# Kernel tuning notes

Measured on AMD Instinct MI355X. Metric: run time of the kernel, lower is better.

Reference implementation:

```python
import jax, jax.numpy as jnp
import numpy as np

N = 50000      # nodes
E = 800000     # edges
FIN = 128      # num_feature
EDIM = 16      # edge_dim
OUT = 64       # out_dim (per-head channels; concat=False averages heads)
H = 4          # heads
SCALE = 1.0 / float(np.sqrt(OUT))


def _layernorm(h, g, b):
    mu = h.mean(-1, keepdims=True)
    var = ((h - mu) ** 2).mean(-1, keepdims=True)
    return (h - mu) * jax.lax.rsqrt(var + 1e-5) * g + b


def _tconv(x, src, dst, ea, Wq, bq, Wk, bk, Wv, bv, We, Ws, bs):
    # PyG TransformerConv, concat=False, root_weight=True, eval mode (no dropout)
    n = x.shape[0]
    q = (x @ Wq + bq).reshape(n, H, OUT)[dst]   # [E,H,D] query at destination
    k = (x @ Wk + bk).reshape(n, H, OUT)[src]   # [E,H,D] key at source
    v = (x @ Wv + bv).reshape(n, H, OUT)[src]   # [E,H,D] value at source
    e = (ea @ We).reshape(-1, H, OUT)           # [E,H,D] edge embedding (no bias)
    logits = jnp.einsum('ehd,ehd->eh', q, k + e) * SCALE   # [E,H]
    # segment softmax over incoming edges of each destination node
    m = jax.lax.stop_gradient(jax.ops.segment_max(logits, dst, num_segments=n))
    a = jnp.exp(logits - m[dst])
    s = jax.ops.segment_sum(a, dst, num_segments=n)
    alpha = a / s[dst]                                     # [E,H]
    agg = jax.ops.segment_sum((v + e) * alpha[..., None], dst, num_segments=n)  # [N,H,D]
    return agg.mean(axis=1) + x @ Ws + bs      # concat=False -> head mean; + skip


def _forward(x, src, dst, ea, p1, p2, p3, g, b):
    h = x
    for p in (p1, p2, p3):
        h = jax.nn.gelu(_layernorm(_tconv(h, src, dst, ea, *p), g, b), approximate=False)
    return h


def setup_inputs() -> dict:
    key = jax.random.key(0)
    ks = iter(jax.random.split(key, 64))
    def nrm(shp, s=0.05):
        return jax.random.normal(next(ks), shp, jnp.float32) * s
    inp = {
        'x': nrm((N, FIN), 1.0),
        'edge_index': jax.random.randint(next(ks), (2, E), 0, N),
        'edge_attr': nrm((E, EDIM), 1.0),
    }
    for l, fin in ((1, FIN), (2, OUT), (3, OUT)):
        inp[f'Wq{l}'] = nrm((fin, H * OUT)); inp[f'bq{l}'] = jnp.zeros((H * OUT,), jnp.float32)
        inp[f'Wk{l}'] = nrm((fin, H * OUT)); inp[f'bk{l}'] = jnp.zeros((H * OUT,), jnp.float32)
        inp[f'Wv{l}'] = nrm((fin, H * OUT)); inp[f'bv{l}'] = jnp.zeros((H * OUT,), jnp.float32)
        inp[f'We{l}'] = nrm((EDIM, H * OUT))
        inp[f'Ws{l}'] = nrm((fin, OUT)); inp[f'bs{l}'] = jnp.zeros((OUT,), jnp.float32)
    inp['ln_g'] = jnp.ones((OUT,), jnp.float32)
    inp['ln_b'] = jnp.zeros((OUT,), jnp.float32)
    return inp


def reference(x, edge_index, edge_attr,
              Wq1, bq1, Wk1, bk1, Wv1, bv1, We1, Ws1, bs1,
              Wq2, bq2, Wk2, bk2, Wv2, bv2, We2, Ws2, bs2,
              Wq3, bq3, Wk3, bk3, Wv3, bv3, We3, Ws3, bs3,
              ln_g, ln_b):
    src, dst = edge_index[0], edge_index[1]
    p1 = (Wq1, bq1, Wk1, bk1, Wv1, bv1, We1, Ws1, bs1)
    p2 = (Wq2, bq2, Wk2, bk2, Wv2, bv2, We2, Ws2, bs2)
    p3 = (Wq3, bq3, Wk3, bk3, Wv3, bv3, We3, Ws3, bs3)
    return _forward(x, src, dst, edge_attr, p1, p2, p3, ln_g, ln_b)
```

## Files before the change

kernel.cpp:

```cpp
#include <hip/hip_runtime.h>
#include <hip/hip_bf16.h>
#include <math.h>

#define NNODES 50000
#define NEDGES 800000
#define HD     256
#define CW     640
#define NTOT   896

typedef __hip_bfloat16 bf16;
typedef unsigned short u16;
typedef unsigned char  u8;
typedef unsigned int   u32;
typedef __attribute__((ext_vector_type(8))) short bf16x8;
typedef __attribute__((ext_vector_type(4))) float f32x4;
typedef __attribute__((ext_vector_type(2))) float f32x2;

__device__ __forceinline__ float lo16f(u32 u) { return __uint_as_float(u << 16); }
__device__ __forceinline__ float hi16f(u32 u) { return __uint_as_float(u & 0xFFFF0000u); }
__device__ __forceinline__ short f2s(float v) { __hip_bfloat16 h = __float2bfloat16(v); return *(short*)&h; }

template<int CTRL>
__device__ __forceinline__ float dppadd(float x) {
    int t = __builtin_amdgcn_update_dpp(0, __float_as_int(x), CTRL, 0xF, 0xF, true);
    return x + __int_as_float(t);
}

__global__ void hist_kernel(const int* __restrict__ dst, int* __restrict__ deg, int E) {
    int e = blockIdx.x * 256 + threadIdx.x;
    if (e < E) atomicAdd(&deg[dst[e]], 1);
}

__global__ void scanA(const int* __restrict__ deg, int* __restrict__ locincl,
                      int* __restrict__ blocksum, int n) {
    int tid = threadIdx.x;
    int i = blockIdx.x * 256 + tid;
    int v = (i < n) ? deg[i] : 0;
    int lane = tid & 63, w = tid >> 6;
    int s = v;
    #pragma unroll
    for (int off = 1; off < 64; off <<= 1) {
        int t = __shfl_up(s, off);
        if (lane >= off) s += t;
    }
    __shared__ int wsum[4];
    if (lane == 63) wsum[w] = s;
    __syncthreads();
    for (int ww = 0; ww < w; ww++) s += wsum[ww];
    if (i < n) locincl[i] = s;
    if (tid == 255) blocksum[blockIdx.x] = s;
}

__global__ void scanB(const int* __restrict__ blocksum, int* __restrict__ blockoff,
                      int nb, int* __restrict__ rowptr, int n) {
    int tid = threadIdx.x;
    int v = (tid < nb) ? blocksum[tid] : 0;
    int lane = tid & 63, w = tid >> 6;
    int s = v;
    #pragma unroll
    for (int off = 1; off < 64; off <<= 1) {
        int t = __shfl_up(s, off);
        if (lane >= off) s += t;
    }
    __shared__ int wsum[4];
    if (lane == 63) wsum[w] = s;
    __syncthreads();
    for (int ww = 0; ww < w; ww++) s += wsum[ww];
    if (tid < nb) blockoff[tid] = s - v;
    if (tid == 255) rowptr[n] = s;
}

__global__ void scanC(const int* __restrict__ deg, const int* __restrict__ locincl,
                      const int* __restrict__ blockoff,
                      int* __restrict__ rowptr, int* __restrict__ cursor, int n) {
    int i = blockIdx.x * 256 + threadIdx.x;
    if (i < n) {
        int ex = locincl[i] - deg[i] + blockoff[blockIdx.x];
        rowptr[i] = ex;
        cursor[i] = ex;
    }
}

__global__ void scatter_kernel(const int* __restrict__ src, const int* __restrict__ dst,
                               int* __restrict__ cursor, int2* __restrict__ csr2, int E) {
    int e = blockIdx.x * 256 + threadIdx.x;
    if (e < E) {
        int d = dst[e];
        int p = atomicAdd(&cursor[d], 1);
        csr2[p] = make_int2(src[e], e);
    }
}

__global__ void pack_all(const float* __restrict__ Wq, const float* __restrict__ bq,
                         const float* __restrict__ Wk, const float* __restrict__ bk,
                         const float* __restrict__ Wv, const float* __restrict__ bv,
                         const float* __restrict__ We,
                         const float* __restrict__ Ws, const float* __restrict__ bs,
                         bf16* __restrict__ Wc, float* __restrict__ b, int K) {
    int n = blockIdx.x, c = threadIdx.x;
    float v, bb;
    if (n < 256)      { v = Wq[(size_t)c * 256 + n];         bb = bq[n]; }
    else if (n < 320) {
        int t = n - 256, h = t >> 4, j = t & 15;
        float s = 0.f, sb = 0.f;
        #pragma unroll 8
        for (int d = 0; d < 64; d++) {
            float wv = We[j * HD + h * 64 + d];
            s += Wq[(size_t)c * 256 + h * 64 + d] * wv;
            sb += bq[h * 64 + d] * wv;
        }
        v = s; bb = sb;
    }
    else if (n < 576) { v = Wv[(size_t)c * 256 + (n - 320)]; bb = bv[n - 320]; }
    else if (n < 640) { v = Ws[(size_t)c * 64  + (n - 576)]; bb = bs[n - 576]; }
    else              { v = Wk[(size_t)c * 256 + (n - 640)]; bb = bk[n - 640]; }
    Wc[(size_t)n * K + c] = __float2bfloat16(v);
    if (c == 0) b[n] = bb;
}

template<typename TA, int K>
__global__ void __launch_bounds__(256) gemm_fused(
    const TA* __restrict__ A, const bf16* __restrict__ Wc, const float* __restrict__ bias,
    bf16* __restrict__ comb, u8* __restrict__ k8)
{
    constexpr int KS  = K / 32;
    constexpr int CPR = K / 8;
    __shared__ short Bl[64 * K];
    int tid = threadIdx.x, w = tid >> 6, lane = tid & 63;
    int cl = lane & 15, aq = lane >> 4;
    int m = blockIdx.x * 64 + w * 16 + cl;
    int rowc = (m < NNODES) ? m : (NNODES - 1);

    bf16x8 af[KS];
    if constexpr (sizeof(TA) == 4) {
        const float* ar = (const float*)A + (size_t)rowc * K;
        #pragma unroll
        for (int ks = 0; ks < KS; ks++) {
            const float4* ap = (const float4*)(ar + ks * 32 + aq * 8);
            float4 f0 = ap[0], f1 = ap[1];
            union { short s[8]; bf16x8 v; } t;
            t.s[0] = f2s(f0.x); t.s[1] = f2s(f0.y); t.s[2] = f2s(f0.z); t.s[3] = f2s(f0.w);
            t.s[4] = f2s(f1.x); t.s[5] = f2s(f1.y); t.s[6] = f2s(f1.z); t.s[7] = f2s(f1.w);
            af[ks] = t.v;
        }
    } else {
        const u16* ar = (const u16*)A + (size_t)rowc * K;
        #pragma unroll
        for (int ks = 0; ks < KS; ks++) af[ks] = *(const bf16x8*)(ar + ks * 32 + aq * 8);
    }

    for (int chunk = 0; chunk < 14; chunk++) {
        int n0 = chunk * 64;
        __syncthreads();
        #pragma unroll
        for (int p = 0; p < CPR / 4; p++) {
            int slot = tid + p * 256;
            int row = slot / CPR, j = slot % CPR;
            *(uint4*)&Bl[row * K + ((j ^ (row & 7)) << 3)] =
                *(const uint4*)((const u16*)Wc + (size_t)(n0 + row) * K + (j << 3));
        }
        __syncthreads();

        f32x4 acc[4] = {};
        #pragma unroll
        for (int t = 0; t < 4; t++) {
            #pragma unroll
            for (int ks = 0; ks < KS; ks++) {
                int g = ((ks * 4 + aq) ^ (cl & 7)) << 3;
                bf16x8 bfr = *(const bf16x8*)&Bl[(t * 16 + cl) * K + g];
                acc[t] = __builtin_amdgcn_mfma_f32_16x16x32_bf16(bfr, af[ks], acc[t], 0, 0, 0);
            }
        }

        if (m < NNODES) {
            #pragma unroll
            for (int t = 0; t < 4; t++) {
                float4 bv = *(const float4*)&bias[n0 + t * 16 + aq * 4];
                float v0 = acc[t][0] + bv.x, v1 = acc[t][1] + bv.y;
                float v2 = acc[t][2] + bv.z, v3 = acc[t][3] + bv.w;
                if (chunk < 10) {
                    u32 lo = (u32)(u16)f2s(v0) | ((u32)(u16)f2s(v1) << 16);
                    u32 hi = (u32)(u16)f2s(v2) | ((u32)(u16)f2s(v3) << 16);
                    *(uint2*)((u16*)comb + (size_t)m * CW + n0 + t * 16 + aq * 4) = make_uint2(lo, hi);
                } else {
                    u32 pk = __builtin_amdgcn_cvt_pk_fp8_f32(v0, v1, 0, false);
                    pk = __builtin_amdgcn_cvt_pk_fp8_f32(v2, v3, pk, true);
                    *(u32*)(k8 + (size_t)m * 256 + (n0 - 640) + t * 16 + aq * 4) = pk;
                }
            }
        }
    }
}

__device__ __forceinline__ void edge_accum(
    u32 s, u32 eid,
    const char* __restrict__ comb_b, const char* __restrict__ k8_b, const char* __restrict__ eattr_b,
    u32 koff, u32 voff, u32 eoff,
    float qf0, float qf1, float qf2, float qf3, float qwe_r,
    float& ss, float& av0, float& av1, float& av2, float& av3, float& ae)
{
    u32   kw = *(const u32*)  (k8_b   + ((s << 8) + koff));
    uint2 vw = *(const uint2*)(comb_b + (s * 1280u + voff));
    float ea = *(const float*)(eattr_b + ((eid << 6) + eoff));
    f32x2 k01 = __builtin_amdgcn_cvt_pk_f32_fp8(kw, false);
    f32x2 k23 = __builtin_amdgcn_cvt_pk_f32_fp8(kw, true);
    float part = qf0 * k01[0] + qf1 * k01[1] + qf2 * k23[0] + qf3 * k23[1] + qwe_r * ea;
    part = dppadd<0xB1>(part);
    part = dppadd<0x4E>(part);
    part = dppadd<0x141>(part);
    part = dppadd<0x140>(part);
    float alpha = __expf(part * 0.125f);
    ss += alpha;
    ae += alpha * ea;
    av0 += alpha * lo16f(vw.x); av1 += alpha * hi16f(vw.x);
    av2 += alpha * lo16f(vw.y); av3 += alpha * hi16f(vw.y);
}

__global__ void __launch_bounds__(256) node_fused(
    const int* __restrict__ rowptr, const int2* __restrict__ csr2,
    const float* __restrict__ eattr, const u16* __restrict__ comb,
    const u8* __restrict__ k8, const float* __restrict__ We,
    const float* __restrict__ lng, const float* __restrict__ lnb,
    bf16* __restrict__ outB, float* __restrict__ outF)
{
    int tid = threadIdx.x, w = tid >> 6, lane = tid & 63;
    int n = blockIdx.x * 4 + w;
    int hg = lane >> 4, j16 = lane & 15, coff = 4 * lane;
    __shared__ float sAV[4][256];
    __shared__ float sAE[4][64];

    const u16* crow = comb + (size_t)n * CW;
    uint2 qv = *(const uint2*)(crow + coff);
    float qf0 = lo16f(qv.x), qf1 = hi16f(qv.x), qf2 = lo16f(qv.y), qf3 = hi16f(qv.y);
    float qwe_r = __uint_as_float((u32)crow[256 + lane] << 16);

    const char* comb_b  = (const char*)comb;
    const char* k8_b    = (const char*)k8;
    const char* eattr_b = (const char*)eattr;
    u32 koff = (u32)coff;
    u32 voff = 640u + ((u32)coff << 1);
    u32 eoff = (u32)j16 << 2;

    int e0 = rowptr[n], e1 = rowptr[n + 1];
    float ss = 0.f, av0 = 0.f, av1 = 0.f, av2 = 0.f, av3 = 0.f, ae = 0.f;

    for (int base = e0; base < e1; base += 64) {
        int cnt = e1 - base; if (cnt > 64) cnt = 64;
        int2 meta = make_int2(0, 0);
        if (lane < cnt) meta = csr2[base + lane];
        int i = 0;
        for (; i + 3 < cnt; i += 4) {
            u32 s0 = __builtin_amdgcn_readlane(meta.x, i);
            u32 q0 = __builtin_amdgcn_readlane(meta.y, i);
            u32 s1 = __builtin_amdgcn_readlane(meta.x, i + 1);
            u32 q1 = __builtin_amdgcn_readlane(meta.y, i + 1);
            u32 s2 = __builtin_amdgcn_readlane(meta.x, i + 2);
            u32 q2 = __builtin_amdgcn_readlane(meta.y, i + 2);
            u32 s3 = __builtin_amdgcn_readlane(meta.x, i + 3);
            u32 q3 = __builtin_amdgcn_readlane(meta.y, i + 3);
            edge_accum(s0, q0, comb_b, k8_b, eattr_b, koff, voff, eoff, qf0, qf1, qf2, qf3, qwe_r, ss, av0, av1, av2, av3, ae);
            edge_accum(s1, q1, comb_b, k8_b, eattr_b, koff, voff, eoff, qf0, qf1, qf2, qf3, qwe_r, ss, av0, av1, av2, av3, ae);
            edge_accum(s2, q2, comb_b, k8_b, eattr_b, koff, voff, eoff, qf0, qf1, qf2, qf3, qwe_r, ss, av0, av1, av2, av3, ae);
            edge_accum(s3, q3, comb_b, k8_b, eattr_b, koff, voff, eoff, qf0, qf1, qf2, qf3, qwe_r, ss, av0, av1, av2, av3, ae);
        }
        for (; i < cnt; ++i) {
            u32 s0 = __builtin_amdgcn_readlane(meta.x, i);
            u32 q0 = __builtin_amdgcn_readlane(meta.y, i);
            edge_accum(s0, q0, comb_b, k8_b, eattr_b, koff, voff, eoff, qf0, qf1, qf2, qf3, qwe_r, ss, av0, av1, av2, av3, ae);
        }
    }

    float inv = (ss > 0.f) ? 1.f / ss : 0.f;
    *(float4*)&sAV[w][coff] = make_float4(av0 * inv, av1 * inv, av2 * inv, av3 * inv);
    sAE[w][lane] = ae * inv;

    int d = lane;
    float val = 0.f;
    #pragma unroll
    for (int h = 0; h < 4; h++) {
        float xv = sAV[w][h * 64 + d];
        #pragma unroll
        for (int j = 0; j < 16; j++) xv += sAE[w][h * 16 + j] * We[j * HD + h * 64 + d];
        val += xv;
    }
    val = val * 0.25f + __uint_as_float((u32)crow[576 + d] << 16);

    float m = val;
    #pragma unroll
    for (int off = 1; off < 64; off <<= 1) m += __shfl_xor(m, off);
    m *= (1.f / 64.f);
    float diff = val - m;
    float vr = diff * diff;
    #pragma unroll
    for (int off = 1; off < 64; off <<= 1) vr += __shfl_xor(vr, off);
    vr *= (1.f / 64.f);
    float y = diff * rsqrtf(vr + 1e-5f) * lng[d] + lnb[d];
    float ge = 0.5f * y * (1.f + erff(y * 0.70710678118654752f));
    if (outF) outF[(size_t)n * 64 + d] = ge;
    else      outB[(size_t)n * 64 + d] = __float2bfloat16(ge);
}

extern "C" void kernel_launch(void* const* d_in, const int* in_sizes, int n_in,
                              void* d_out, int out_size, void* d_ws, size_t ws_size,
                              hipStream_t stream)
{
    const float* x     = (const float*)d_in[0];
    const int*   eidx  = (const int*)d_in[1];
    const float* eattr = (const float*)d_in[2];
    struct P { const float *Wq,*bq,*Wk,*bk,*Wv,*bv,*We,*Ws,*bs; };
    P p[3];
    for (int l = 0; l < 3; l++) {
        int base = 3 + l * 9;
        p[l].Wq = (const float*)d_in[base + 0]; p[l].bq = (const float*)d_in[base + 1];
        p[l].Wk = (const float*)d_in[base + 2]; p[l].bk = (const float*)d_in[base + 3];
        p[l].Wv = (const float*)d_in[base + 4]; p[l].bv = (const float*)d_in[base + 5];
        p[l].We = (const float*)d_in[base + 6];
        p[l].Ws = (const float*)d_in[base + 7]; p[l].bs = (const float*)d_in[base + 8];
    }
    const float* lng = (const float*)d_in[30];
    const float* lnb = (const float*)d_in[31];

    char* ws = (char*)d_ws;
    size_t off = 0;
    auto alloc = [&](size_t bytes) { void* pp = ws + off; off += (bytes + 255) & ~(size_t)255; return pp; };
    int*   rowptr   = (int*)  alloc((NNODES + 1) * 4);
    int*   cursor   = (int*)  alloc(NNODES * 4);
    int*   deg      = (int*)  alloc(NNODES * 4);
    int*   blocksum = (int*)  alloc(256 * 4);
    int*   blockoff = (int*)  alloc(256 * 4);
    int2*  csr2     = (int2*) alloc((size_t)NEDGES * 8);
    bf16*  hbuf     = (bf16*) alloc((size_t)NNODES * 64 * 2);
    bf16*  comb     = (bf16*) alloc((size_t)NNODES * CW * 2);
    u8*    k8       = (u8*)   alloc((size_t)NNODES * 256);
    bf16*  Wc       = (bf16*) alloc((size_t)NTOT * 128 * 2);
    float* b896     = (float*)alloc(NTOT * 4);
    (void)ws_size;

    const int* srcArr = eidx;
    const int* dstArr = eidx + NEDGES;

    int NB = (NNODES + 255) / 256;
    (void)hipMemsetAsync(deg, 0, NNODES * 4, stream);
    hist_kernel<<<(NEDGES + 255) / 256, 256, 0, stream>>>(dstArr, deg, NEDGES);
    scanA<<<NB, 256, 0, stream>>>(deg, cursor, blocksum, NNODES);
    scanB<<<1, 256, 0, stream>>>(blocksum, blockoff, NB, rowptr, NNODES);
    scanC<<<NB, 256, 0, stream>>>(deg, cursor, blockoff, rowptr, cursor, NNODES);
    scatter_kernel<<<(NEDGES + 255) / 256, 256, 0, stream>>>(srcArr, dstArr, cursor, csr2, NEDGES);

    int gm = (NNODES + 63) / 64;
    int fins[3] = {128, 64, 64};

    const void* hin = x;
    for (int l = 0; l < 3; l++) {
        int FIN = fins[l];
        pack_all<<<NTOT, FIN, 0, stream>>>(p[l].Wq, p[l].bq, p[l].Wk, p[l].bk,
                                           p[l].Wv, p[l].bv, p[l].We, p[l].Ws, p[l].bs,
                                           Wc, b896, FIN);
        if (l == 0) gemm_fused<float, 128><<<gm, 256, 0, stream>>>((const float*)hin, Wc, b896, comb, k8);
        else        gemm_fused<bf16,  64><<<gm, 256, 0, stream>>>((const bf16*)hin,  Wc, b896, comb, k8);
        node_fused<<<NNODES / 4, 256, 0, stream>>>(rowptr, csr2, eattr, (const u16*)comb, k8,
            p[l].We, lng, lnb, (l == 2) ? nullptr : hbuf, (l == 2) ? (float*)d_out : nullptr);
        hin = hbuf;
    }
}
```

Measured before the change: 688.5 us.

## Split V into separate buffer, stage GEMM output via LDS, prefetch edges

Moves the value projection into its own contiguous 512-byte-per-node buffer and reorders the combined row so the skip projection sits right after Q and q·We. GEMM epilogue outputs go through a swizzled LDS tile, so each thread issues coalesced 16-byte global stores. The weight chunk for the next step is register-prefetched while the current one computes. The softmax scale and log2(e) are folded into the Q weights so the edge loop can use a raw exp2. The edge loop now reads CSR entries with a rolling 4-edge prefetch instead of wave-wide loads plus readlane broadcasts. This costs extra LDS, one more barrier per chunk and more register pressure.

```diff
diff --git a/kernel.cpp b/kernel.cpp
--- a/kernel.cpp
+++ b/kernel.cpp
@@ -5,13 +5,15 @@
 #define NNODES 50000
 #define NEDGES 800000
 #define HD     256
-#define CW     640
+#define CW     448
 #define NTOT   896
+#define QS     0.18033688011112042f
 
 typedef __hip_bfloat16 bf16;
 typedef unsigned short u16;
 typedef unsigned char  u8;
 typedef unsigned int   u32;
+typedef unsigned long long u64;
 typedef __attribute__((ext_vector_type(8))) short bf16x8;
 typedef __attribute__((ext_vector_type(4))) float f32x4;
 typedef __attribute__((ext_vector_type(2))) float f32x2;
@@ -99,7 +101,7 @@
                          bf16* __restrict__ Wc, float* __restrict__ b, int K) {
     int n = blockIdx.x, c = threadIdx.x;
     float v, bb;
-    if (n < 256)      { v = Wq[(size_t)c * 256 + n];         bb = bq[n]; }
+    if (n < 256)      { v = Wq[(size_t)c * 256 + n] * QS;    bb = bq[n] * QS; }
     else if (n < 320) {
         int t = n - 256, h = t >> 4, j = t & 15;
         float s = 0.f, sb = 0.f;
@@ -109,10 +111,10 @@
             s += Wq[(size_t)c * 256 + h * 64 + d] * wv;
             sb += bq[h * 64 + d] * wv;
         }
-        v = s; bb = sb;
-    }
-    else if (n < 576) { v = Wv[(size_t)c * 256 + (n - 320)]; bb = bv[n - 320]; }
-    else if (n < 640) { v = Ws[(size_t)c * 64  + (n - 576)]; bb = bs[n - 576]; }
+        v = s * QS; bb = sb * QS;
+    }
+    else if (n < 384) { v = Ws[(size_t)c * 64  + (n - 320)]; bb = bs[n - 320]; }
+    else if (n < 640) { v = Wv[(size_t)c * 256 + (n - 384)]; bb = bv[n - 384]; }
     else              { v = Wk[(size_t)c * 256 + (n - 640)]; bb = bk[n - 640]; }
     Wc[(size_t)n * K + c] = __float2bfloat16(v);
     if (c == 0) b[n] = bb;
@@ -121,14 +123,17 @@
 template<typename TA, int K>
 __global__ void __launch_bounds__(256) gemm_fused(
     const TA* __restrict__ A, const bf16* __restrict__ Wc, const float* __restrict__ bias,
-    bf16* __restrict__ comb, u8* __restrict__ k8)
+    bf16* __restrict__ comb, bf16* __restrict__ vbuf, u8* __restrict__ k8)
 {
     constexpr int KS  = K / 32;
     constexpr int CPR = K / 8;
+    constexpr int SLD = CPR / 4;
     __shared__ short Bl[64 * K];
+    __shared__ u8    Tr[64 * 128];
     int tid = threadIdx.x, w = tid >> 6, lane = tid & 63;
     int cl = lane & 15, aq = lane >> 4;
-    int m = blockIdx.x * 64 + w * 16 + cl;
+    int m0 = blockIdx.x * 64;
+    int m  = m0 + w * 16 + cl;
     int rowc = (m < NNODES) ? m : (NNODES - 1);
 
     bf16x8 af[KS];
@@ -149,16 +154,26 @@
         for (int ks = 0; ks < KS; ks++) af[ks] = *(const bf16x8*)(ar + ks * 32 + aq * 8);
     }
 
-    for (int chunk = 0; chunk < 14; chunk++) {
-        int n0 = chunk * 64;
-        __syncthreads();
-        #pragma unroll
-        for (int p = 0; p < CPR / 4; p++) {
+    uint4 sreg[SLD];
+    auto SLOAD = [&](int chunk) {
+        #pragma unroll
+        for (int p = 0; p < SLD; p++) {
             int slot = tid + p * 256;
             int row = slot / CPR, j = slot % CPR;
-            *(uint4*)&Bl[row * K + ((j ^ (row & 7)) << 3)] =
-                *(const uint4*)((const u16*)Wc + (size_t)(n0 + row) * K + (j << 3));
-        }
+            sreg[p] = *(const uint4*)((const u16*)Wc + (size_t)(chunk * 64 + row) * K + (j << 3));
+        }
+    };
+    SLOAD(0);
+
+    for (int chunk = 0; chunk < 14; chunk++) {
+        __syncthreads();
+        #pragma unroll
+        for (int p = 0; p < SLD; p++) {
+            int slot = tid + p * 256;
+            int row = slot / CPR, j = slot % CPR;
+            *(uint4*)&Bl[row * K + ((j ^ (row & 7)) << 3)] = sreg[p];
+        }
+        if (chunk < 13) SLOAD(chunk + 1);
         __syncthreads();
 
         f32x4 acc[4] = {};
@@ -172,55 +187,61 @@
             }
         }
 
-        if (m < NNODES) {
+        int r = w * 16 + cl;
+        if (chunk < 10) {
             #pragma unroll
             for (int t = 0; t < 4; t++) {
-                float4 bv = *(const float4*)&bias[n0 + t * 16 + aq * 4];
-                float v0 = acc[t][0] + bv.x, v1 = acc[t][1] + bv.y;
-                float v2 = acc[t][2] + bv.z, v3 = acc[t][3] + bv.w;
-                if (chunk < 10) {
-                    u32 lo = (u32)(u16)f2s(v0) | ((u32)(u16)f2s(v1) << 16);
-                    u32 hi = (u32)(u16)f2s(v2) | ((u32)(u16)f2s(v3) << 16);
-                    *(uint2*)((u16*)comb + (size_t)m * CW + n0 + t * 16 + aq * 4) = make_uint2(lo, hi);
-                } else {
-                    u32 pk = __builtin_amdgcn_cvt_pk_fp8_f32(v0, v1, 0, false);
-                    pk = __builtin_amdgcn_cvt_pk_fp8_f32(v2, v3, pk, true);
-                    *(u32*)(k8 + (size_t)m * 256 + (n0 - 640) + t * 16 + aq * 4) = pk;
+                float4 bv = *(const float4*)&bias[chunk * 64 + t * 16 + aq * 4];
+                u32 lo = (u32)(u16)f2s(acc[t][0] + bv.x) | ((u32)(u16)f2s(acc[t][1] + bv.y) << 16);
+                u32 hi = (u32)(u16)f2s(acc[t][2] + bv.z) | ((u32)(u16)f2s(acc[t][3] + bv.w) << 16);
+                *(uint2*)&Tr[r * 128 + (((t * 4 + aq) ^ (r & 15)) << 3)] = make_uint2(lo, hi);
+            }
+        } else {
+            #pragma unroll
+            for (int t = 0; t < 4; t++) {
+                float4 bv = *(const float4*)&bias[chunk * 64 + t * 16 + aq * 4];
+                u32 pk = __builtin_amdgcn_cvt_pk_fp8_f32(acc[t][0] + bv.x, acc[t][1] + bv.y, 0, false);
+                pk = __builtin_amdgcn_cvt_pk_fp8_f32(acc[t][2] + bv.z, acc[t][3] + bv.w, pk, true);
+                *(u32*)&Tr[r * 64 + (((t * 4 + aq) ^ (r & 15)) << 2)] = pk;
+            }
+        }
+        __syncthreads();
+
+        int r2 = tid >> 2, q = tid & 3;
+        int gr = m0 + r2;
+        if (gr < NNODES) {
+            if (chunk < 10) {
+                union { u32 d[4]; uint4 v; } o0, o1;
+                #pragma unroll
+                for (int j = 0; j < 4; j++) {
+                    int g = ((q * 4 + j) ^ (r2 & 15)) << 3;
+                    uint2 dv = *(const uint2*)&Tr[r2 * 128 + g];
+                    if (j < 2) { o0.d[2 * j] = dv.x; o0.d[2 * j + 1] = dv.y; }
+                    else       { o1.d[2 * (j - 2)] = dv.x; o1.d[2 * (j - 2) + 1] = dv.y; }
                 }
+                char* dst;
+                if (chunk < 6) dst = (char*)comb + (size_t)gr * (CW * 2) + chunk * 128;
+                else           dst = (char*)vbuf + (size_t)gr * 512 + (chunk - 6) * 128;
+                *(uint4*)(dst + q * 32)      = o0.v;
+                *(uint4*)(dst + q * 32 + 16) = o1.v;
+            } else {
+                union { u32 d[4]; uint4 v; } o;
+                #pragma unroll
+                for (int j = 0; j < 4; j++) {
+                    int g = ((q * 4 + j) ^ (r2 & 15)) << 2;
+                    o.d[j] = *(const u32*)&Tr[r2 * 64 + g];
+                }
+                *(uint4*)((char*)k8 + (size_t)gr * 256 + (chunk - 10) * 64 + q * 16) = o.v;
             }
         }
     }
-}
-
-__device__ __forceinline__ void edge_accum(
-    u32 s, u32 eid,
-    const char* __restrict__ comb_b, const char* __restrict__ k8_b, const char* __restrict__ eattr_b,
-    u32 koff, u32 voff, u32 eoff,
-    float qf0, float qf1, float qf2, float qf3, float qwe_r,
-    float& ss, float& av0, float& av1, float& av2, float& av3, float& ae)
-{
-    u32   kw = *(const u32*)  (k8_b   + ((s << 8) + koff));
-    uint2 vw = *(const uint2*)(comb_b + (s * 1280u + voff));
-    float ea = *(const float*)(eattr_b + ((eid << 6) + eoff));
-    f32x2 k01 = __builtin_amdgcn_cvt_pk_f32_fp8(kw, false);
-    f32x2 k23 = __builtin_amdgcn_cvt_pk_f32_fp8(kw, true);
-    float part = qf0 * k01[0] + qf1 * k01[1] + qf2 * k23[0] + qf3 * k23[1] + qwe_r * ea;
-    part = dppadd<0xB1>(part);
-    part = dppadd<0x4E>(part);
-    part = dppadd<0x141>(part);
-    part = dppadd<0x140>(part);
-    float alpha = __expf(part * 0.125f);
-    ss += alpha;
-    ae += alpha * ea;
-    av0 += alpha * lo16f(vw.x); av1 += alpha * hi16f(vw.x);
-    av2 += alpha * lo16f(vw.y); av3 += alpha * hi16f(vw.y);
 }
 
 __global__ void __launch_bounds__(256) node_fused(
     const int* __restrict__ rowptr, const int2* __restrict__ csr2,
     const float* __restrict__ eattr, const u16* __restrict__ comb,
-    const u8* __restrict__ k8, const float* __restrict__ We,
-    const float* __restrict__ lng, const float* __restrict__ lnb,
+    const u16* __restrict__ vbuf, const u8* __restrict__ k8,
+    const float* __restrict__ We, const float* __restrict__ lng, const float* __restrict__ lnb,
     bf16* __restrict__ outB, float* __restrict__ outF)
 {
     int tid = threadIdx.x, w = tid >> 6, lane = tid & 63;
@@ -234,41 +255,42 @@
     float qf0 = lo16f(qv.x), qf1 = hi16f(qv.x), qf2 = lo16f(qv.y), qf3 = hi16f(qv.y);
     float qwe_r = __uint_as_float((u32)crow[256 + lane] << 16);
 
-    const char* comb_b  = (const char*)comb;
-    const char* k8_b    = (const char*)k8;
-    const char* eattr_b = (const char*)eattr;
-    u32 koff = (u32)coff;
-    u32 voff = 640u + ((u32)coff << 1);
-    u32 eoff = (u32)j16 << 2;
-
-    int e0 = rowptr[n], e1 = rowptr[n + 1];
+    int e0 = __builtin_amdgcn_readfirstlane(rowptr[n]);
+    int e1 = __builtin_amdgcn_readfirstlane(rowptr[n + 1]);
+
     float ss = 0.f, av0 = 0.f, av1 = 0.f, av2 = 0.f, av3 = 0.f, ae = 0.f;
-
-    for (int base = e0; base < e1; base += 64) {
-        int cnt = e1 - base; if (cnt > 64) cnt = 64;
-        int2 meta = make_int2(0, 0);
-        if (lane < cnt) meta = csr2[base + lane];
-        int i = 0;
-        for (; i + 3 < cnt; i += 4) {
-            u32 s0 = __builtin_amdgcn_readlane(meta.x, i);
-            u32 q0 = __builtin_amdgcn_readlane(meta.y, i);
-            u32 s1 = __builtin_amdgcn_readlane(meta.x, i + 1);
-            u32 q1 = __builtin_amdgcn_readlane(meta.y, i + 1);
-            u32 s2 = __builtin_amdgcn_readlane(meta.x, i + 2);
-            u32 q2 = __builtin_amdgcn_readlane(meta.y, i + 2);
-            u32 s3 = __builtin_amdgcn_readlane(meta.x, i + 3);
-            u32 q3 = __builtin_amdgcn_readlane(meta.y, i + 3);
-            edge_accum(s0, q0, comb_b, k8_b, eattr_b, koff, voff, eoff, qf0, qf1, qf2, qf3, qwe_r, ss, av0, av1, av2, av3, ae);
-            edge_accum(s1, q1, comb_b, k8_b, eattr_b, koff, voff, eoff, qf0, qf1, qf2, qf3, qwe_r, ss, av0, av1, av2, av3, ae);
-            edge_accum(s2, q2, comb_b, k8_b, eattr_b, koff, voff, eoff, qf0, qf1, qf2, qf3, qwe_r, ss, av0, av1, av2, av3, ae);
-            edge_accum(s3, q3, comb_b, k8_b, eattr_b, koff, voff, eoff, qf0, qf1, qf2, qf3, qwe_r, ss, av0, av1, av2, av3, ae);
-        }
-        for (; i < cnt; ++i) {
-            u32 s0 = __builtin_amdgcn_readlane(meta.x, i);
-            u32 q0 = __builtin_amdgcn_readlane(meta.y, i);
-            edge_accum(s0, q0, comb_b, k8_b, eattr_b, koff, voff, eoff, qf0, qf1, qf2, qf3, qwe_r, ss, av0, av1, av2, av3, ae);
-        }
-    }
+    u32 vo = (u32)coff * 2u;
+    u32 eo = (u32)j16 * 4u;
+
+    auto EDGE = [&](int2 me) {
+        u32 s = (u32)me.x, eid = (u32)me.y;
+        u32   kw = *(const u32*)  ((const char*)k8    + ((s << 8) + (u32)coff));
+        uint2 vw = *(const uint2*)((const char*)vbuf  + ((s << 9) + vo));
+        float ea = *(const float*)((const char*)eattr + ((eid << 6) + eo));
+        f32x2 k01 = __builtin_amdgcn_cvt_pk_f32_fp8(kw, false);
+        f32x2 k23 = __builtin_amdgcn_cvt_pk_f32_fp8(kw, true);
+        float part = qf0 * k01[0] + qf1 * k01[1] + qf2 * k23[0] + qf3 * k23[1] + qwe_r * ea;
+        part = dppadd<0xB1>(part);
+        part = dppadd<0x4E>(part);
+        part = dppadd<0x141>(part);
+        part = dppadd<0x140>(part);
+        float alpha = __builtin_amdgcn_exp2f(part);
+        ss += alpha;
+        ae += alpha * ea;
+        av0 += alpha * lo16f(vw.x); av1 += alpha * hi16f(vw.x);
+        av2 += alpha * lo16f(vw.y); av3 += alpha * hi16f(vw.y);
+    };
+
+    int i = e0;
+    int2 c0 = make_int2(0, 0), c1 = c0, c2 = c0, c3 = c0;
+    if (i + 3 < e1) { c0 = csr2[i]; c1 = csr2[i + 1]; c2 = csr2[i + 2]; c3 = csr2[i + 3]; }
+    for (; i + 7 < e1; i += 4) {
+        int2 p0 = csr2[i + 4], p1 = csr2[i + 5], p2 = csr2[i + 6], p3 = csr2[i + 7];
+        EDGE(c0); EDGE(c1); EDGE(c2); EDGE(c3);
+        c0 = p0; c1 = p1; c2 = p2; c3 = p3;
+    }
+    if (i + 3 < e1) { EDGE(c0); EDGE(c1); EDGE(c2); EDGE(c3); i += 4; }
+    for (; i < e1; ++i) { int2 cc = csr2[i]; EDGE(cc); }
 
     float inv = (ss > 0.f) ? 1.f / ss : 0.f;
     *(float4*)&sAV[w][coff] = make_float4(av0 * inv, av1 * inv, av2 * inv, av3 * inv);
@@ -283,7 +305,7 @@
         for (int j = 0; j < 16; j++) xv += sAE[w][h * 16 + j] * We[j * HD + h * 64 + d];
         val += xv;
     }
-    val = val * 0.25f + __uint_as_float((u32)crow[576 + d] << 16);
+    val = val * 0.25f + __uint_as_float((u32)crow[320 + d] << 16);
 
     float m = val;
     #pragma unroll
@@ -331,6 +353,7 @@
     int2*  csr2     = (int2*) alloc((size_t)NEDGES * 8);
     bf16*  hbuf     = (bf16*) alloc((size_t)NNODES * 64 * 2);
     bf16*  comb     = (bf16*) alloc((size_t)NNODES * CW * 2);
+    bf16*  vbuf     = (bf16*) alloc((size_t)NNODES * 256 * 2);
     u8*    k8       = (u8*)   alloc((size_t)NNODES * 256);
     bf16*  Wc       = (bf16*) alloc((size_t)NTOT * 128 * 2);
     float* b896     = (float*)alloc(NTOT * 4);
@@ -356,10 +379,11 @@
         pack_all<<<NTOT, FIN, 0, stream>>>(p[l].Wq, p[l].bq, p[l].Wk, p[l].bk,
                                            p[l].Wv, p[l].bv, p[l].We, p[l].Ws, p[l].bs,
                                            Wc, b896, FIN);
-        if (l == 0) gemm_fused<float, 128><<<gm, 256, 0, stream>>>((const float*)hin, Wc, b896, comb, k8);
-        else        gemm_fused<bf16,  64><<<gm, 256, 0, stream>>>((const bf16*)hin,  Wc, b896, comb, k8);
-        node_fused<<<NNODES / 4, 256, 0, stream>>>(rowptr, csr2, eattr, (const u16*)comb, k8,
-            p[l].We, lng, lnb, (l == 2) ? nullptr : hbuf, (l == 2) ? (float*)d_out : nullptr);
+        if (l == 0) gemm_fused<float, 128><<<gm, 256, 0, stream>>>((const float*)hin, Wc, b896, comb, vbuf, k8);
+        else        gemm_fused<bf16,  64><<<gm, 256, 0, stream>>>((const bf16*)hin,  Wc, b896, comb, vbuf, k8);
+        node_fused<<<NNODES / 4, 256, 0, stream>>>(rowptr, csr2, eattr, (const u16*)comb,
+            (const u16*)vbuf, k8, p[l].We, lng, lnb,
+            (l == 2) ? nullptr : hbuf, (l == 2) ? (float*)d_out : nullptr);
         hin = hbuf;
     }
 }
```

New measurement: 733.4 us. 1.07x slower.
